# Performance work log

Hardware: AMD Instinct MI355X
Metric: run time of the kernel (lower is better)

Reference implementation:

```python
import jax, jax.numpy as jnp
from jax import lax
import numpy as np

LOG2PI = float(np.log(2.0 * np.pi))
FMIN = float(np.finfo(np.float32).min)


def seq_mask(lengths, maxlen):
    # [B, maxlen] float32
    return (jnp.arange(maxlen)[None] < lengths[:, None]).astype(jnp.float32)


def monotonic_alignment_search(ll, attnmask):
    """Faithful port of GlowTTS.monotonic_alignment_search.
    ll, attnmask: [B, T, S] float32. Returns [B, T, S] float32.
    Note: replicates the source exactly, including stacking backtracked rows
    in descending-j (append) order before masking, as written in the TF code.
    """
    B, T, S = ll.shape
    x_range = jnp.arange(S)[None]  # [1, S]

    def fwd(prob, j_and_ll):
        j, ll_j = j_and_ll  # ll_j: [B, S]
        prev = jnp.pad(prob, ((0, 0), (1, 0)), constant_values=-jnp.inf)[:, :-1]
        max_mask = prob >= prev                       # [B, S] bool
        prob_max = jnp.where(max_mask, prob, prev)
        prob_new = jnp.where(x_range <= j, prob_max + ll_j, FMIN)
        return prob_new, max_mask

    _, direction = lax.scan(fwd, jnp.zeros((B, S), jnp.float32),
                            (jnp.arange(T), jnp.transpose(ll, (1, 0, 2))))
    direction = jnp.transpose(direction, (1, 0, 2)).astype(jnp.int32)  # [B, T, S]
    direction = jnp.where(attnmask.astype(bool), direction, 1)

    index = attnmask[:, 0].sum(axis=-1).astype(jnp.int32) - 1  # [B]
    brange = jnp.arange(B)

    def bwd(index, j):
        attn_j = jax.nn.one_hot(index, S, dtype=jnp.float32)  # drops index<0 like scatter_nd
        d = direction[brange, j, index]                       # [B]
        return index + d - 1, attn_j

    _, attn = lax.scan(bwd, index, jnp.arange(T)[::-1])
    attn = jnp.transpose(attn, (1, 0, 2))  # [B, T, S], rows in append order
    return attn * attnmask


def setup_inputs() -> dict:
    key = jax.random.key(0)
    k1, k2, k3, k4, k5 = jax.random.split(key, 5)
    B, T, S, C = 32, 1200, 384, 160
    latent = jax.random.normal(k1, (B, T, C), dtype=jnp.float32)
    mean = jax.random.normal(k2, (B, S, C), dtype=jnp.float32)
    logdur = jax.random.normal(k3, (B, S), dtype=jnp.float32)
    textlen = jax.random.randint(k4, (B,), S // 2, S + 1).astype(jnp.int32)
    mellen = jax.random.randint(k5, (B,), T // 2, T + 1).astype(jnp.int32)
    return {"latent": latent, "mean": mean, "logdur": logdur,
            "textlen": textlen, "mellen": mellen}


def reference(latent, mean, logdur, textlen, mellen):
    B, T, C = latent.shape
    S = mean.shape[1]
    mask = seq_mask(textlen, S)     # [B, S]
    melmask = seq_mask(mellen, T)   # [B, T]
    attnmask = melmask[..., None] * mask[:, None]  # [B, T, S]

    # pairwise squared distance (cdist via matmul + reduce_sum)
    dist = (jnp.sum(jnp.square(latent), axis=-1, keepdims=True)
            - 2.0 * jnp.einsum('btc,bsc->bts', latent, mean)
            + jnp.sum(jnp.square(mean), axis=-1)[:, None])
    ll = -0.5 * (LOG2PI + dist) * attnmask

    attn = lax.stop_gradient(monotonic_alignment_search(ll, attnmask))
    aligned = jnp.einsum('bts,bsc->btc', attn, mean)  # [B, T, C]

    # negative log-likelihood (dlogdet of the flow omitted: constant here)
    nll = 0.5 * (LOG2PI + jnp.sum(jnp.square(latent - aligned), axis=(1, 2)))
    nll = jnp.mean(nll / (mellen * C).astype(jnp.float32))

    gtdur = jnp.log(jnp.maximum(jnp.sum(attn, axis=1), 1e-05)) * mask
    durloss = jnp.sum(jnp.square(logdur - gtdur), axis=-1) / mellen.astype(jnp.float32)
    durloss = jnp.mean(durloss)

    loss = nll + durloss
    return loss, attn
```

## Files before the change

kernel.cpp:

```cpp
#include <hip/hip_runtime.h>
#include <math.h>

#define LOG2PI 1.8378770664093453f
#define F32MIN (-3.4028234663852886e38f)
#define SMAX 384
#define NW 38

__global__ __launch_bounds__(64) void k_sums(
    const float* __restrict__ latent, const float* __restrict__ mean,
    float* __restrict__ lx2, float* __restrict__ lm2, int BT, int BS, int C) {
  int row = blockIdx.x;
  int lane = threadIdx.x;
  const float* src;
  float* dst;
  if (row < BT) { src = latent + (size_t)row * C; dst = lx2 + row; }
  else          { src = mean + (size_t)(row - BT) * C; dst = lm2 + (row - BT); }
  float s = 0.f;
  for (int c = lane; c < C; c += 64) { float v = src[c]; s += v * v; }
  #pragma unroll
  for (int off = 32; off; off >>= 1) s += __shfl_down(s, off);
  if (lane == 0) *dst = s;
}

__global__ __launch_bounds__(256) void k_scores(
    const float* __restrict__ latent, const float* __restrict__ mean,
    const float* __restrict__ lx2, const float* __restrict__ lm2,
    const int* __restrict__ textlen, const int* __restrict__ mellen,
    float* __restrict__ ll, int T, int S, int C) {
  int b  = blockIdx.z;
  int t0 = blockIdx.x * 64;
  int s0 = blockIdx.y * 64;
  int mel = mellen[b], txt = textlen[b];
  int tid = threadIdx.x;
  int ty = tid >> 4, tx = tid & 15;
  float* out = ll + ((size_t)b * T + t0) * S + s0;

  if (t0 >= mel || s0 >= txt) {
    float4 z = make_float4(0.f, 0.f, 0.f, 0.f);
    #pragma unroll
    for (int i = 0; i < 4; ++i) {
      int tl = ty * 4 + i;
      if (t0 + tl < T) *(float4*)(out + (size_t)tl * S + tx * 4) = z;
    }
    return;
  }

  __shared__ float At[16][64];
  __shared__ float Bt[16][64];
  float acc[4][4] = {};

  const float* Ab = latent + ((size_t)b * T + t0) * C;
  const float* Bb = mean + ((size_t)b * S + s0) * C;

  for (int kk = 0; kk < C; kk += 16) {
    int r  = tid >> 2;
    int cg = tid & 3;
    float4 a = (t0 + r < T) ? *(const float4*)(Ab + (size_t)r * C + kk + cg * 4)
                            : make_float4(0.f, 0.f, 0.f, 0.f);
    float4 bm = *(const float4*)(Bb + (size_t)r * C + kk + cg * 4);
    At[cg * 4 + 0][r] = a.x;  At[cg * 4 + 1][r] = a.y;
    At[cg * 4 + 2][r] = a.z;  At[cg * 4 + 3][r] = a.w;
    Bt[cg * 4 + 0][r] = bm.x; Bt[cg * 4 + 1][r] = bm.y;
    Bt[cg * 4 + 2][r] = bm.z; Bt[cg * 4 + 3][r] = bm.w;
    __syncthreads();
    #pragma unroll
    for (int k = 0; k < 16; ++k) {
      float4 a4 = *(const float4*)&At[k][ty * 4];
      float4 b4 = *(const float4*)&Bt[k][tx * 4];
      float av[4] = {a4.x, a4.y, a4.z, a4.w};
      float bv[4] = {b4.x, b4.y, b4.z, b4.w};
      #pragma unroll
      for (int i = 0; i < 4; ++i)
        #pragma unroll
        for (int j = 0; j < 4; ++j)
          acc[i][j] = fmaf(av[i], bv[j], acc[i][j]);
    }
    __syncthreads();
  }

  #pragma unroll
  for (int i = 0; i < 4; ++i) {
    int t = t0 + ty * 4 + i;
    if (t >= T) continue;
    float lx = lx2[(size_t)b * T + t];
    float4 o;
    float* po = &o.x;
    #pragma unroll
    for (int j = 0; j < 4; ++j) {
      int s = s0 + tx * 4 + j;
      float d = lx - 2.f * acc[i][j] + lm2[(size_t)b * S + s];
      float v = -0.5f * (LOG2PI + d);
      po[j] = (t < mel && s < txt) ? v : 0.f;
    }
    *(float4*)(out + (size_t)(ty * 4 + i) * S + tx * 4) = o;
  }
}

__device__ __forceinline__ float dpp_shr1_neginf(float x) {
  int r = __builtin_amdgcn_update_dpp(
      __float_as_int(-INFINITY), __float_as_int(x),
      0x138 , 0xf, 0xf, false);
  return __int_as_float(r);
}

template <bool MASKED>
__device__ __forceinline__ void mas_step(
    int t, int sbase, int r, const float2 A0, const float2 A1, const float2 A2,
    float& p0, float& p1, float& p2, float& p3, float& p4, float& p5,
    unsigned& a0, unsigned& a1, unsigned& a2, unsigned& a3, unsigned& a4,
    unsigned& a5) {
  float l0 = A0.x, l1 = A0.y, l2 = A1.x, l3 = A1.y, l4 = A2.x, l5 = A2.y;
  float pm1 = dpp_shr1_neginf(p5);
  bool c0 = p0 >= pm1, c1 = p1 >= p0, c2 = p2 >= p1;
  bool c3 = p3 >= p2,  c4 = p4 >= p3, c5 = p5 >= p4;
  float m0 = c0 ? p0 : pm1, m1 = c1 ? p1 : p0, m2 = c2 ? p2 : p1;
  float m3 = c3 ? p3 : p2,  m4 = c4 ? p4 : p3, m5 = c5 ? p5 : p4;
  a0 |= (unsigned)c0 << r; a1 |= (unsigned)c1 << r; a2 |= (unsigned)c2 << r;
  a3 |= (unsigned)c3 << r; a4 |= (unsigned)c4 << r; a5 |= (unsigned)c5 << r;
  if (MASKED) {
    p0 = (sbase + 0 <= t) ? m0 + l0 : F32MIN;
    p1 = (sbase + 1 <= t) ? m1 + l1 : F32MIN;
    p2 = (sbase + 2 <= t) ? m2 + l2 : F32MIN;
    p3 = (sbase + 3 <= t) ? m3 + l3 : F32MIN;
    p4 = (sbase + 4 <= t) ? m4 + l4 : F32MIN;
    p5 = (sbase + 5 <= t) ? m5 + l5 : F32MIN;
  } else {
    p0 = m0 + l0; p1 = m1 + l1; p2 = m2 + l2;
    p3 = m3 + l3; p4 = m4 + l4; p5 = m5 + l5;
  }
}

template <bool MASKED, int ROWS>
__device__ __forceinline__ void scan_chunk_lds(
    const float* __restrict__ rcur, int t0, int sbase,
    float& p0, float& p1, float& p2, float& p3, float& p4, float& p5,
    unsigned* __restrict__ dirT, int cw) {
  unsigned a0 = 0, a1 = 0, a2 = 0, a3 = 0, a4 = 0, a5 = 0;
  const float2* q = (const float2*)(rcur + sbase);
  float2 A0 = q[0], A1 = q[1], A2 = q[2];
  #pragma unroll 1
  for (int r = 0; r < ROWS; r += 2) {
    const float2* qb = q + (size_t)(r + 1) * 192;
    float2 B0 = qb[0], B1 = qb[1], B2 = qb[2];
    mas_step<MASKED>(t0 + r, sbase, r, A0, A1, A2,
                     p0, p1, p2, p3, p4, p5, a0, a1, a2, a3, a4, a5);
    int rn = (r + 2 < ROWS) ? (r + 2) : (ROWS - 1);
    const float2* qa = q + (size_t)rn * 192;
    A0 = qa[0]; A1 = qa[1]; A2 = qa[2];
    mas_step<MASKED>(t0 + r + 1, sbase, r + 1, B0, B1, B2,
                     p0, p1, p2, p3, p4, p5, a0, a1, a2, a3, a4, a5);
  }
  unsigned* dcol = dirT + (unsigned)sbase * NW + cw;
  dcol[0] = a0; dcol[NW] = a1; dcol[2 * NW] = a2;
  dcol[3 * NW] = a3; dcol[4 * NW] = a4; dcol[5 * NW] = a5;
}

__global__ __launch_bounds__(256, 1) void k_scan(
    const float* __restrict__ ll, const int* __restrict__ textlen,
    const int* __restrict__ mellen, int* __restrict__ pathidx, int T, int S) {
  int b = blockIdx.x;
  int tid = threadIdx.x;
  int lane = tid & 63;
  __shared__ float rows[2][32][SMAX];
  __shared__ unsigned dirT[SMAX * NW];

  const float* llb = ll + (size_t)b * T * S;
  int mel = mellen[b], txt = textlen[b];
  int sbase = lane * 6;
  int nfull = T / 32;
  int nch = (T + 31) / 32;
  float p0 = 0.f, p1 = 0.f, p2 = 0.f, p3 = 0.f, p4 = 0.f, p5 = 0.f;

  if (tid >= 64) {
    int lid = tid - 64;
    const float4* g = (const float4*)llb;
    float4* d = (float4*)&rows[0][0][0];
    #pragma unroll
    for (int k = 0; k < 16; ++k) d[k * 192 + lid] = g[k * 192 + lid];
  }
  __syncthreads();

  for (int c = 0; c < nch; ++c) {
    if (tid >= 64) {
      int nxt = c + 1;
      if (nxt < nch) {
        int lid = tid - 64;
        const float4* g = (const float4*)(llb + (size_t)nxt * 32 * S);
        float4* d = (float4*)&rows[nxt & 1][0][0];
        if (nxt < nfull) {
          float4 stg[16];
          #pragma unroll
          for (int k = 0; k < 16; ++k) stg[k] = g[k * 192 + lid];
          #pragma unroll
          for (int k = 0; k < 16; ++k) d[k * 192 + lid] = stg[k];
        } else {
          float4 stg[8];
          #pragma unroll
          for (int k = 0; k < 8; ++k) stg[k] = g[k * 192 + lid];
          #pragma unroll
          for (int k = 0; k < 8; ++k) d[k * 192 + lid] = stg[k];
        }
      }
    } else {
      const float* rc = &rows[c & 1][0][0];
      int t0 = c * 32;
      if (c < nfull) {
        if (t0 < S)
          scan_chunk_lds<true, 32>(rc, t0, sbase, p0, p1, p2, p3, p4, p5, dirT, c);
        else
          scan_chunk_lds<false, 32>(rc, t0, sbase, p0, p1, p2, p3, p4, p5, dirT, c);
      } else {
        scan_chunk_lds<false, 16>(rc, t0, sbase, p0, p1, p2, p3, p4, p5, dirT, c);
      }
    }
    __syncthreads();
  }

  if (tid >= 64) return;

  size_t base = (size_t)b * T;
  int k0 = T - mel;
  for (int k = lane; k < k0; k += 64) pathidx[base + k] = txt - 1;

  if (lane == 0) {
    int i = txt - 1;
    int j = mel - 1;
    unsigned w = ~0u;
    bool reload = true;
    for (int k = k0; k < T; ++k) {
      pathidx[base + k] = i;
      if (reload) {
        int ii = (i < 0) ? i + S : i;
        ii = (ii < 0) ? 0 : ii;
        w = (ii < txt) ? dirT[ii * NW + (j >> 5)] : ~0u;
      }
      int d = (int)((w >> (j & 31)) & 1u);
      reload = (d == 0) | ((j & 31) == 0);
      i += d - 1;
      --j;
    }
  }
}

__global__ __launch_bounds__(256) void k_scatter(
    float* __restrict__ attn, const int* __restrict__ pathidx,
    const int* __restrict__ textlen, const int* __restrict__ mellen,
    int B, int T, int S) {
  size_t idx = ((size_t)blockIdx.x * blockDim.x + threadIdx.x) * 4;
  size_t total = (size_t)B * T * S;
  if (idx >= total) return;
  int s = (int)(idx % S);
  size_t row = idx / S;
  int b = (int)(row / T);
  int k = (int)(row % T);
  int pi = pathidx[row];
  int mel = mellen[b], txt = textlen[b];
  float4 o = make_float4(0.f, 0.f, 0.f, 0.f);
  if (k < mel && pi >= 0 && pi < S && pi < txt && pi >= s && pi < s + 4)
    (&o.x)[pi - s] = 1.f;
  *(float4*)(attn + idx) = o;
}

__global__ __launch_bounds__(256) void k_rowloss(
    const float* __restrict__ latent, const float* __restrict__ mean,
    const int* __restrict__ pathidx, const int* __restrict__ textlen,
    const int* __restrict__ mellen, float* __restrict__ rowsum,
    int T, int S, int C) {
  int row = blockIdx.x * 4 + (threadIdx.x >> 6);
  int lane = threadIdx.x & 63;
  int b = row / T, k = row % T;
  int pi = pathidx[row];
  int mel = mellen[b], txt = textlen[b];
  bool on = (k < mel) && (pi >= 0) && (pi < S) && (pi < txt);
  const float* L = latent + (size_t)row * C;
  const float* M = mean + ((size_t)b * S + (on ? pi : 0)) * C;
  float s = 0.f;
  for (int c = lane; c < C; c += 64) {
    float d = L[c] - (on ? M[c] : 0.f);
    s += d * d;
  }
  #pragma unroll
  for (int off = 32; off; off >>= 1) s += __shfl_down(s, off);
  if (lane == 0) rowsum[row] = s;
}

__global__ __launch_bounds__(256) void k_batch(
    const float* __restrict__ rowsum, const int* __restrict__ pathidx,
    const float* __restrict__ logdur, const int* __restrict__ textlen,
    const int* __restrict__ mellen, float* __restrict__ nllc,
    float* __restrict__ durc, int T, int S, int C) {
  int b = blockIdx.x;
  int tid = threadIdx.x;
  __shared__ int hist[512];
  __shared__ float red[256];
  int mel = mellen[b], txt = textlen[b];
  for (int s = tid; s < S; s += 256) hist[s] = 0;
  __syncthreads();
  for (int k = tid; k < T; k += 256) {
    int pi = pathidx[(size_t)b * T + k];
    if (k < mel && pi >= 0 && pi < S && pi < txt) atomicAdd(&hist[pi], 1);
  }
  __syncthreads();
  float part = 0.f;
  for (int s = tid; s < S; s += 256) {
    float cnt = (float)hist[s];
    float gt = logf(fmaxf(cnt, 1e-5f));
    gt = (s < txt) ? gt : 0.f;
    float d = logdur[(size_t)b * S + s] - gt;
    part += d * d;
  }
  red[tid] = part; __syncthreads();
  #pragma unroll
  for (int off = 128; off; off >>= 1) {
    if (tid < off) red[tid] += red[tid + off];
    __syncthreads();
  }
  if (tid == 0) durc[b] = red[0] / (float)mel;
  __syncthreads();
  part = 0.f;
  for (int k = tid; k < T; k += 256) part += rowsum[(size_t)b * T + k];
  red[tid] = part; __syncthreads();
  #pragma unroll
  for (int off = 128; off; off >>= 1) {
    if (tid < off) red[tid] += red[tid + off];
    __syncthreads();
  }
  if (tid == 0) nllc[b] = 0.5f * (LOG2PI + red[0]) / ((float)mel * (float)C);
}

__global__ __launch_bounds__(64) void k_final(
    const float* __restrict__ nllc, const float* __restrict__ durc,
    float* __restrict__ out, int B) {
  int lane = threadIdx.x;
  float v = (lane < B) ? (nllc[lane] + durc[lane]) : 0.f;
  #pragma unroll
  for (int off = 32; off; off >>= 1) v += __shfl_down(v, off);
  if (lane == 0) out[0] = v / (float)B;
}

extern "C" void kernel_launch(void* const* d_in, const int* in_sizes, int n_in,
                              void* d_out, int out_size, void* d_ws, size_t ws_size,
                              hipStream_t stream) {
  (void)n_in; (void)out_size; (void)ws_size;
  const float* latent = (const float*)d_in[0];
  const float* mean   = (const float*)d_in[1];
  const float* logdur = (const float*)d_in[2];
  const int*   textlen = (const int*)d_in[3];
  const int*   mellen  = (const int*)d_in[4];

  int B = in_sizes[3];
  int S = in_sizes[2] / B;
  int C = in_sizes[1] / (B * S);
  int T = in_sizes[0] / (B * C);

  float* out = (float*)d_out;
  float* ll = out + 1;

  char* ws = (char*)d_ws;
  float* lx2    = (float*)ws;
  float* lm2    = lx2 + (size_t)B * T;
  int*   pathidx = (int*)(lm2 + (size_t)B * S);
  float* rowsum  = (float*)(pathidx + (size_t)B * T);
  float* nllc    = rowsum + (size_t)B * T;
  float* durc    = nllc + B;

  k_sums<<<B * T + B * S, 64, 0, stream>>>(latent, mean, lx2, lm2, B * T, B * S, C);

  dim3 g2((T + 63) / 64, (S + 63) / 64, B);
  k_scores<<<g2, 256, 0, stream>>>(latent, mean, lx2, lm2, textlen, mellen, ll, T, S, C);

  k_scan<<<B, 256, 0, stream>>>(ll, textlen, mellen, pathidx, T, S);

  size_t total = (size_t)B * T * S;
  k_scatter<<<(int)((total / 4 + 255) / 256), 256, 0, stream>>>(ll, pathidx, textlen, mellen, B, T, S);

  k_rowloss<<<(B * T) / 4, 256, 0, stream>>>(latent, mean, pathidx, textlen, mellen, rowsum, T, S, C);

  k_batch<<<B, 256, 0, stream>>>(rowsum, pathidx, logdur, textlen, mellen, nllc, durc, T, S, C);

  k_final<<<1, 64, 0, stream>>>(nllc, durc, out, B);
}
```

Baseline: 324.9 us.

## Skip zero-fill and post-mel chunks, branchless MAS step with specialized LDS buffers

```diff
diff --git a/kernel.cpp b/kernel.cpp
--- a/kernel.cpp
+++ b/kernel.cpp
@@ -35,15 +35,7 @@
   int ty = tid >> 4, tx = tid & 15;
   float* out = ll + ((size_t)b * T + t0) * S + s0;
 
-  if (t0 >= mel || s0 >= txt) {
-    float4 z = make_float4(0.f, 0.f, 0.f, 0.f);
-    #pragma unroll
-    for (int i = 0; i < 4; ++i) {
-      int tl = ty * 4 + i;
-      if (t0 + tl < T) *(float4*)(out + (size_t)tl * S + tx * 4) = z;
-    }
-    return;
-  }
+  if (t0 >= mel || s0 >= txt || s0 > t0 + 63) return;
 
   __shared__ float At[16][64];
   __shared__ float Bt[16][64];
@@ -103,56 +95,8 @@
   return __int_as_float(r);
 }
 
-template <bool MASKED>
-__device__ __forceinline__ void mas_step(
-    int t, int sbase, int r, const float2 A0, const float2 A1, const float2 A2,
-    float& p0, float& p1, float& p2, float& p3, float& p4, float& p5,
-    unsigned& a0, unsigned& a1, unsigned& a2, unsigned& a3, unsigned& a4,
-    unsigned& a5) {
-  float l0 = A0.x, l1 = A0.y, l2 = A1.x, l3 = A1.y, l4 = A2.x, l5 = A2.y;
-  float pm1 = dpp_shr1_neginf(p5);
-  bool c0 = p0 >= pm1, c1 = p1 >= p0, c2 = p2 >= p1;
-  bool c3 = p3 >= p2,  c4 = p4 >= p3, c5 = p5 >= p4;
-  float m0 = c0 ? p0 : pm1, m1 = c1 ? p1 : p0, m2 = c2 ? p2 : p1;
-  float m3 = c3 ? p3 : p2,  m4 = c4 ? p4 : p3, m5 = c5 ? p5 : p4;
-  a0 |= (unsigned)c0 << r; a1 |= (unsigned)c1 << r; a2 |= (unsigned)c2 << r;
-  a3 |= (unsigned)c3 << r; a4 |= (unsigned)c4 << r; a5 |= (unsigned)c5 << r;
-  if (MASKED) {
-    p0 = (sbase + 0 <= t) ? m0 + l0 : F32MIN;
-    p1 = (sbase + 1 <= t) ? m1 + l1 : F32MIN;
-    p2 = (sbase + 2 <= t) ? m2 + l2 : F32MIN;
-    p3 = (sbase + 3 <= t) ? m3 + l3 : F32MIN;
-    p4 = (sbase + 4 <= t) ? m4 + l4 : F32MIN;
-    p5 = (sbase + 5 <= t) ? m5 + l5 : F32MIN;
-  } else {
-    p0 = m0 + l0; p1 = m1 + l1; p2 = m2 + l2;
-    p3 = m3 + l3; p4 = m4 + l4; p5 = m5 + l5;
-  }
-}
-
-template <bool MASKED, int ROWS>
-__device__ __forceinline__ void scan_chunk_lds(
-    const float* __restrict__ rcur, int t0, int sbase,
-    float& p0, float& p1, float& p2, float& p3, float& p4, float& p5,
-    unsigned* __restrict__ dirT, int cw) {
-  unsigned a0 = 0, a1 = 0, a2 = 0, a3 = 0, a4 = 0, a5 = 0;
-  const float2* q = (const float2*)(rcur + sbase);
-  float2 A0 = q[0], A1 = q[1], A2 = q[2];
-  #pragma unroll 1
-  for (int r = 0; r < ROWS; r += 2) {
-    const float2* qb = q + (size_t)(r + 1) * 192;
-    float2 B0 = qb[0], B1 = qb[1], B2 = qb[2];
-    mas_step<MASKED>(t0 + r, sbase, r, A0, A1, A2,
-                     p0, p1, p2, p3, p4, p5, a0, a1, a2, a3, a4, a5);
-    int rn = (r + 2 < ROWS) ? (r + 2) : (ROWS - 1);
-    const float2* qa = q + (size_t)rn * 192;
-    A0 = qa[0]; A1 = qa[1]; A2 = qa[2];
-    mas_step<MASKED>(t0 + r + 1, sbase, r + 1, B0, B1, B2,
-                     p0, p1, p2, p3, p4, p5, a0, a1, a2, a3, a4, a5);
-  }
-  unsigned* dcol = dirT + (unsigned)sbase * NW + cw;
-  dcol[0] = a0; dcol[NW] = a1; dcol[2 * NW] = a2;
-  dcol[3 * NW] = a3; dcol[4 * NW] = a4; dcol[5 * NW] = a5;
+__device__ __forceinline__ float selmask(float v, int m) {
+  return __int_as_float((__float_as_int(v) & ~m) | ((int)0xFF7FFFFF & m));
 }
 
 __global__ __launch_bounds__(256, 1) void k_scan(
@@ -169,6 +113,8 @@
   int sbase = lane * 6;
   int nfull = T / 32;
   int nch = (T + 31) / 32;
+  int nchb = (mel + 31) / 32;
+  if (nchb > nch) nchb = nch;
   float p0 = 0.f, p1 = 0.f, p2 = 0.f, p3 = 0.f, p4 = 0.f, p5 = 0.f;
 
   if (tid >= 64) {
@@ -180,10 +126,63 @@
   }
   __syncthreads();
 
-  for (int c = 0; c < nch; ++c) {
+#define LROW(X0, X1, X2, CB, R) do { \
+    X0 = *(const float2*)&rows[CB][R][sbase]; \
+    X1 = *(const float2*)&rows[CB][R][sbase + 2]; \
+    X2 = *(const float2*)&rows[CB][R][sbase + 4]; } while (0)
+
+#define MAS_STEP(MASKEDV, T_, R_, X0, X1, X2) do { \
+    float pm1 = dpp_shr1_neginf(p5); \
+    unsigned s0b = __float_as_uint(p0 - pm1) >> 31; \
+    unsigned s1b = __float_as_uint(p1 - p0)  >> 31; \
+    unsigned s2b = __float_as_uint(p2 - p1)  >> 31; \
+    unsigned s3b = __float_as_uint(p3 - p2)  >> 31; \
+    unsigned s4b = __float_as_uint(p4 - p3)  >> 31; \
+    unsigned s5b = __float_as_uint(p5 - p4)  >> 31; \
+    n0 |= s0b << (R_); n1 |= s1b << (R_); n2 |= s2b << (R_); \
+    n3 |= s3b << (R_); n4 |= s4b << (R_); n5 |= s5b << (R_); \
+    float v0 = fmaxf(p0, pm1) + X0.x; \
+    float v1 = fmaxf(p1, p0) + X0.y; \
+    float v2 = fmaxf(p2, p1) + X1.x; \
+    float v3 = fmaxf(p3, p2) + X1.y; \
+    float v4 = fmaxf(p4, p3) + X2.x; \
+    float v5 = fmaxf(p5, p4) + X2.y; \
+    if (MASKEDV) { \
+      int base_ = (T_) - sbase; \
+      p0 = selmask(v0, (base_ - 0) >> 31); \
+      p1 = selmask(v1, (base_ - 1) >> 31); \
+      p2 = selmask(v2, (base_ - 2) >> 31); \
+      p3 = selmask(v3, (base_ - 3) >> 31); \
+      p4 = selmask(v4, (base_ - 4) >> 31); \
+      p5 = selmask(v5, (base_ - 5) >> 31); \
+    } else { \
+      p0 = v0; p1 = v1; p2 = v2; p3 = v3; p4 = v4; p5 = v5; \
+    } } while (0)
+
+#define SCANCHUNK(MASKEDV, ROWS, CB, T0, CW) do { \
+    unsigned n0 = 0, n1 = 0, n2 = 0, n3 = 0, n4 = 0, n5 = 0; \
+    float2 A0, A1, A2, B0, B1, B2; \
+    LROW(A0, A1, A2, CB, 0); \
+    _Pragma("unroll 1") \
+    for (int r = 0; r < (ROWS); r += 2) { \
+      LROW(B0, B1, B2, CB, r + 1); \
+      MAS_STEP(MASKEDV, (T0) + r, r, A0, A1, A2); \
+      { int rn = (r + 2 < (ROWS)) ? (r + 2) : ((ROWS) - 1); \
+        LROW(A0, A1, A2, CB, rn); } \
+      MAS_STEP(MASKEDV, (T0) + r + 1, r + 1, B0, B1, B2); \
+    } \
+    dirT[(unsigned)sbase * NW + (CW)] = ~n0; \
+    dirT[(unsigned)(sbase + 1) * NW + (CW)] = ~n1; \
+    dirT[(unsigned)(sbase + 2) * NW + (CW)] = ~n2; \
+    dirT[(unsigned)(sbase + 3) * NW + (CW)] = ~n3; \
+    dirT[(unsigned)(sbase + 4) * NW + (CW)] = ~n4; \
+    dirT[(unsigned)(sbase + 5) * NW + (CW)] = ~n5; \
+  } while (0)
+
+  for (int c = 0; c < nchb; ++c) {
     if (tid >= 64) {
       int nxt = c + 1;
-      if (nxt < nch) {
+      if (nxt < nchb) {
         int lid = tid - 64;
         const float4* g = (const float4*)(llb + (size_t)nxt * 32 * S);
         float4* d = (float4*)&rows[nxt & 1][0][0];
@@ -202,19 +201,24 @@
         }
       }
     } else {
-      const float* rc = &rows[c & 1][0][0];
+      int cb = c & 1;
       int t0 = c * 32;
-      if (c < nfull) {
-        if (t0 < S)
-          scan_chunk_lds<true, 32>(rc, t0, sbase, p0, p1, p2, p3, p4, p5, dirT, c);
-        else
-          scan_chunk_lds<false, 32>(rc, t0, sbase, p0, p1, p2, p3, p4, p5, dirT, c);
+      if (c < 12) {
+        if (cb == 0) SCANCHUNK(true, 32, 0, t0, c);
+        else         SCANCHUNK(true, 32, 1, t0, c);
+      } else if (c < nfull) {
+        if (cb == 0) SCANCHUNK(false, 32, 0, t0, c);
+        else         SCANCHUNK(false, 32, 1, t0, c);
       } else {
-        scan_chunk_lds<false, 16>(rc, t0, sbase, p0, p1, p2, p3, p4, p5, dirT, c);
+        if (cb == 0) SCANCHUNK(false, 16, 0, t0, c);
+        else         SCANCHUNK(false, 16, 1, t0, c);
       }
     }
     __syncthreads();
   }
+#undef SCANCHUNK
+#undef MAS_STEP
+#undef LROW
 
   if (tid >= 64) return;
 
```

Result: no change. 327.1 us (+0.7%).
